# Kernel tuning notes

Hardware: AMD Instinct MI355X
Metric: run time of the kernel (lower is better)

Reference implementation:

```python
import jax, jax.numpy as jnp
import numpy as np

B, C, H, W = 8, 512, 64, 64
NUMS, V_C = 1024, 512
RATE = 0.999


def _normalize(x):
    # matches torch F.normalize(dim=-1, eps=1e-12)
    return x / jnp.clip(jnp.linalg.norm(x, axis=-1, keepdims=True), 1e-12)


def setup_inputs() -> dict:
    key = jax.random.key(0)
    k1, k2, k3 = jax.random.split(key, 3)
    return {
        "x": jax.random.normal(k1, (B, C, H, W), dtype=jnp.float32),
        "noise_feature": jax.random.normal(k2, (NUMS, C), dtype=jnp.float32),
        "std": jax.random.normal(k3, (NUMS, V_C), dtype=jnp.float32),
    }


def reference(x, noise_feature, std):
    b, c, h, w = x.shape
    # (b,c,h,w) -> (n,c)
    xf = jnp.transpose(x, (0, 2, 3, 1)).reshape(-1, c)
    m = jax.lax.stop_gradient(noise_feature)  # torch uses .data (no grad)
    xn = _normalize(xf)
    mn = _normalize(m)
    score = xn @ mn.T  # (n, k) cosine similarities

    # EMA codebook update (training path, update_flag=True)
    xd = jax.lax.stop_gradient(xf)
    embed_ind = jnp.argmax(score, axis=1)  # (n,)
    # segment_sum == x.T @ one_hot(ind), transposed; avoids dense one-hot GEMM
    embed_sum = jax.ops.segment_sum(xd, embed_ind, num_segments=NUMS)  # (k, c)
    counts = jax.ops.segment_sum(jnp.ones((xd.shape[0],), xd.dtype), embed_ind,
                                 num_segments=NUMS)  # (k,)
    embed_mean = embed_sum / (counts[:, None] + 1e-6)
    new_m = m * RATE + embed_mean * (1.0 - RATE)

    mn2 = _normalize(new_m)
    score2 = xn @ mn2.T  # (n, k)
    soft_label = jax.nn.softmax(score2, axis=1)
    out = (soft_label @ std).reshape(b, h, w, V_C)
    return out, score2
```

## Files before the change

kernel.cpp:

```cpp
#include <hip/hip_runtime.h>
#include <stdint.h>

#define NROWS 32768
#define CDIM  512
#define KCODES 1024
#define VC    512
#define LDP 72

typedef unsigned short u16;
typedef unsigned long long u64;
using bf16x8 = __attribute__((ext_vector_type(8))) __bf16;
using f32x4  = __attribute__((ext_vector_type(4))) float;

__device__ __forceinline__ float bf2f(u16 u){
  union { unsigned int i; float f; } x; x.i = ((unsigned int)u) << 16; return x.f;
}
__device__ __forceinline__ u16 f2bf(float f){
  union { float f; unsigned int i; } x; x.f = f;
  unsigned int u = x.i;
  u += 0x7fffu + ((u >> 16) & 1u);
  return (u16)(u >> 16);
}
__device__ __forceinline__ unsigned int pack2(u16 lo, u16 hi){
  return (unsigned int)lo | ((unsigned int)hi << 16);
}
__device__ __forceinline__ unsigned int fkey(float f){
  unsigned int u = __float_as_uint(f);
  return (u & 0x80000000u) ? ~u : (u | 0x80000000u);
}
__device__ __forceinline__ f32x4 mfma16(bf16x8 a, bf16x8 b, f32x4 c){
  return __builtin_amdgcn_mfma_f32_16x16x32_bf16(a, b, c, 0, 0, 0);
}
__device__ __forceinline__ void gload_lds16(const void* g, void* l){
  __builtin_amdgcn_global_load_lds(
      (const __attribute__((address_space(1))) unsigned int*)g,
      (__attribute__((address_space(3))) unsigned int*)l, 16, 0, 0);
}

__global__ __launch_bounds__(256) void k_transpose_x(const float* __restrict__ x,
                                                     u16* __restrict__ xf,
                                                     float* __restrict__ rsum){
  __shared__ float tile[64 * 64];
  int b  = blockIdx.z;
  int p0 = blockIdx.x * 64;
  int c0 = blockIdx.y * 64;
  int t  = threadIdx.x;
  const float* xb = x + (size_t)b * CDIM * 4096 + (size_t)c0 * 4096 + p0;

  int pl4 = (t & 15) * 4;
#pragma unroll
  for (int i = 0; i < 4; i++){
    int cl = i * 16 + (t >> 4);
    float4 v = *(const float4*)(xb + (size_t)cl * 4096 + pl4);
    *(float4*)(tile + cl * 64 + (pl4 ^ (cl & 0x38))) = v;
  }
  __syncthreads();

  int cl0 = (t & 7) * 8;
#pragma unroll
  for (int pass = 0; pass < 2; pass++){
    int pl = pass * 32 + (t >> 3);
    float v[8]; float s = 0.f;
#pragma unroll
    for (int j = 0; j < 8; j++){
      v[j] = tile[(cl0 + j) * 64 + (pl ^ cl0)];
      s += v[j] * v[j];
    }
    uint4 o;
    o.x = pack2(f2bf(v[0]), f2bf(v[1]));
    o.y = pack2(f2bf(v[2]), f2bf(v[3]));
    o.z = pack2(f2bf(v[4]), f2bf(v[5]));
    o.w = pack2(f2bf(v[6]), f2bf(v[7]));
    *(uint4*)(xf + (size_t)(b * 4096 + p0 + pl) * CDIM + c0 + cl0) = o;
    s += __shfl_xor(s, 1, 64);
    s += __shfl_xor(s, 2, 64);
    s += __shfl_xor(s, 4, 64);
    if ((t & 7) == 0) atomicAdd(rsum + b * 4096 + p0 + pl, s);
  }
}

__global__ __launch_bounds__(256) void k_prep(const float* __restrict__ in,
                                              u16* __restrict__ mn,
                                              const float* __restrict__ sd,
                                              u16* __restrict__ stdT){
  int t = threadIdx.x;
  if (blockIdx.x < 256){
    int row  = blockIdx.x * 4 + (t >> 6);
    int lane = t & 63;
    const float* r = in + (size_t)row * CDIM;
    float v[8]; float s = 0.f;
#pragma unroll
    for (int i = 0; i < 8; i++){ v[i] = r[lane + i * 64]; s += v[i] * v[i]; }
#pragma unroll
    for (int off = 32; off; off >>= 1) s += __shfl_xor(s, off, 64);
    float inv = 1.0f / fmaxf(sqrtf(s), 1e-12f);
#pragma unroll
    for (int i = 0; i < 8; i++) mn[(size_t)row * CDIM + lane + i * 64] = f2bf(v[i] * inv);
  } else {
    __shared__ float tile[32][33];
    int bid = blockIdx.x - 256;
    int k0 = (bid & 31) * 32;
    int v0 = (bid >> 5) * 32;
    int tx = t & 31, ty = t >> 5;
#pragma unroll
    for (int i = 0; i < 4; i++)
      tile[ty + i * 8][tx] = sd[(size_t)(k0 + ty + i * 8) * VC + v0 + tx];
    __syncthreads();
#pragma unroll
    for (int i = 0; i < 4; i++)
      stdT[(size_t)(v0 + ty + i * 8) * KCODES + k0 + tx] = f2bf(tile[tx][ty + i * 8]);
  }
}

__global__ __launch_bounds__(512, 4) void k_gemm1_am(const u16* __restrict__ xf,
                                                     const u16* __restrict__ mn,
                                                     u64* __restrict__ packed){
  __shared__ __align__(16) u16 As[256 * 64];
  __shared__ __align__(16) u16 Bs[128 * 64];
  int tid  = threadIdx.x;
  int wave = tid >> 6, lane = tid & 63;
  int wr = wave >> 1, wc = wave & 1;
  int quad = lane >> 4, l15 = lane & 15;
  int c0 = blockIdx.x * 128, r0 = blockIdx.y * 256;

  int srow = lane >> 3, schunk = lane & 7;
  const u16* ag = xf + (size_t)(r0 + wave * 8 + srow) * CDIM + schunk * 8;
  const u16* bg = mn + (size_t)(c0 + wave * 8 + srow) * CDIM + schunk * 8;
  u16* adst = As + wave * 8 * 64;
  u16* bdst = Bs + wave * 8 * 64;

  f32x4 acc[4][4];
#pragma unroll
  for (int rt = 0; rt < 4; rt++)
#pragma unroll
    for (int ct = 0; ct < 4; ct++) acc[rt][ct] = (f32x4)(0.f);

  for (int k0 = 0; k0 < CDIM; k0 += 64){
#pragma unroll
    for (int i = 0; i < 4; i++)
      gload_lds16(ag + (size_t)(i * 64) * CDIM + k0, adst + i * 64 * 64);
#pragma unroll
    for (int j = 0; j < 2; j++)
      gload_lds16(bg + (size_t)(j * 64) * CDIM + k0, bdst + j * 64 * 64);
    __syncthreads();
#pragma unroll
    for (int ks = 0; ks < 2; ks++){
      bf16x8 af[4], bfr[4];
#pragma unroll
      for (int rt = 0; rt < 4; rt++)
        af[rt] = *(const bf16x8*)(As + (wr * 64 + rt * 16 + l15) * 64 + ks * 32 + quad * 8);
#pragma unroll
      for (int ct = 0; ct < 4; ct++)
        bfr[ct] = *(const bf16x8*)(Bs + (wc * 64 + ct * 16 + l15) * 64 + ks * 32 + quad * 8);
#pragma unroll
      for (int rt = 0; rt < 4; rt++)
#pragma unroll
        for (int ct = 0; ct < 4; ct++)
          acc[rt][ct] = mfma16(af[rt], bfr[ct], acc[rt][ct]);
    }
    __syncthreads();
  }

#pragma unroll
  for (int rt = 0; rt < 4; rt++){
#pragma unroll
    for (int q = 0; q < 4; q++){
      float bv = acc[rt][0][q];
      int   bc = c0 + wc * 64 + l15;
#pragma unroll
      for (int ct = 1; ct < 4; ct++){
        float v = acc[rt][ct][q];
        int   c = c0 + wc * 64 + ct * 16 + l15;
        if (v > bv){ bv = v; bc = c; }
      }
#pragma unroll
      for (int off = 1; off <= 8; off <<= 1){
        float ov = __shfl_xor(bv, off, 64);
        int   oc = __shfl_xor(bc, off, 64);
        if (ov > bv || (ov == bv && oc < bc)){ bv = ov; bc = oc; }
      }
      if (l15 == 0){
        int rg = r0 + wr * 64 + rt * 16 + quad * 4 + q;
        u64 key = ((u64)fkey(bv) << 32) | (unsigned int)(~(unsigned int)bc);
        atomicMax(packed + rg, key);
      }
    }
  }
}

__global__ __launch_bounds__(256) void k_gather(const u64* __restrict__ packed,
                                                const u16* __restrict__ xf,
                                                float* __restrict__ esum,
                                                float* __restrict__ counts){
  __shared__ float part[4][CDIM];
  __shared__ int   wcnt[4];
  int code = blockIdx.x;
  int tid = threadIdx.x, wave = tid >> 6, lane = tid & 63;
  float acc[8] = {0,0,0,0,0,0,0,0};
  int cnt = 0;
  for (int base = wave * 64; base < NROWS; base += 256){
    u64 pk = packed[base + lane];
    int cl = (int)(~(unsigned int)(pk & 0xffffffffull)) & (KCODES - 1);
    int match = (cl == code);
    u64 mask = __ballot(match);
    cnt += (int)__popcll(mask);
    while (mask){
      int b = __ffsll((long long)mask) - 1;
      mask &= mask - 1;
      int rr = base + b;
      uint4 v = *(const uint4*)(xf + (size_t)rr * CDIM + lane * 8);
      unsigned int w[4] = {v.x, v.y, v.z, v.w};
#pragma unroll
      for (int i = 0; i < 4; i++){
        acc[2 * i]     += bf2f((u16)(w[i] & 0xffffu));
        acc[2 * i + 1] += bf2f((u16)(w[i] >> 16));
      }
    }
  }
#pragma unroll
  for (int j = 0; j < 8; j++) part[wave][lane * 8 + j] = acc[j];
  if (lane == 0) wcnt[wave] = cnt;
  __syncthreads();
  for (int c = tid; c < CDIM; c += 256)
    esum[(size_t)code * CDIM + c] = part[0][c] + part[1][c] + part[2][c] + part[3][c];
  if (tid == 0) counts[code] = (float)(wcnt[0] + wcnt[1] + wcnt[2] + wcnt[3]);
}

__global__ __launch_bounds__(256) void k_newm(const float* __restrict__ m,
                                              const float* __restrict__ esum,
                                              const float* __restrict__ counts,
                                              u16* __restrict__ mn2){
  int row  = blockIdx.x * 4 + (threadIdx.x >> 6);
  int lane = threadIdx.x & 63;
  float cnt = counts[row];
  float sc  = 0.001f / (cnt + 1e-6f);
  float v[8]; float s = 0.f;
#pragma unroll
  for (int i = 0; i < 8; i++){
    int c = lane + i * 64;
    v[i] = m[(size_t)row * CDIM + c] * 0.999f + esum[(size_t)row * CDIM + c] * sc;
    s += v[i] * v[i];
  }
#pragma unroll
  for (int off = 32; off; off >>= 1) s += __shfl_xor(s, off, 64);
  float inv = 1.0f / fmaxf(sqrtf(s), 1e-12f);
#pragma unroll
  for (int i = 0; i < 8; i++) mn2[(size_t)row * CDIM + lane + i * 64] = f2bf(v[i] * inv);
}

__global__ __launch_bounds__(512, 4) void k_gemm2(const u16* __restrict__ xf,
                                                  const u16* __restrict__ mn2,
                                                  const float* __restrict__ rsum,
                                                  float* __restrict__ score2,
                                                  float* __restrict__ pmax,
                                                  float* __restrict__ psum){
  __shared__ __align__(16) u16 As[256 * 64];
  __shared__ __align__(16) u16 Bs[128 * 64];
  int tid  = threadIdx.x;
  int wave = tid >> 6, lane = tid & 63;
  int wr = wave >> 1, wc = wave & 1;
  int quad = lane >> 4, l15 = lane & 15;
  int c0 = blockIdx.x * 128, r0 = blockIdx.y * 256;

  int srow = lane >> 3, schunk = lane & 7;
  const u16* ag = xf  + (size_t)(r0 + wave * 8 + srow) * CDIM + schunk * 8;
  const u16* bg = mn2 + (size_t)(c0 + wave * 8 + srow) * CDIM + schunk * 8;
  u16* adst = As + wave * 8 * 64;
  u16* bdst = Bs + wave * 8 * 64;

  f32x4 acc[4][4];
#pragma unroll
  for (int rt = 0; rt < 4; rt++)
#pragma unroll
    for (int ct = 0; ct < 4; ct++) acc[rt][ct] = (f32x4)(0.f);

  for (int k0 = 0; k0 < CDIM; k0 += 64){
#pragma unroll
    for (int i = 0; i < 4; i++)
      gload_lds16(ag + (size_t)(i * 64) * CDIM + k0, adst + i * 64 * 64);
#pragma unroll
    for (int j = 0; j < 2; j++)
      gload_lds16(bg + (size_t)(j * 64) * CDIM + k0, bdst + j * 64 * 64);
    __syncthreads();
#pragma unroll
    for (int ks = 0; ks < 2; ks++){
      bf16x8 af[4], bfr[4];
#pragma unroll
      for (int rt = 0; rt < 4; rt++)
        af[rt] = *(const bf16x8*)(As + (wr * 64 + rt * 16 + l15) * 64 + ks * 32 + quad * 8);
#pragma unroll
      for (int ct = 0; ct < 4; ct++)
        bfr[ct] = *(const bf16x8*)(Bs + (wc * 64 + ct * 16 + l15) * 64 + ks * 32 + quad * 8);
#pragma unroll
      for (int rt = 0; rt < 4; rt++)
#pragma unroll
        for (int ct = 0; ct < 4; ct++)
          acc[rt][ct] = mfma16(af[rt], bfr[ct], acc[rt][ct]);
    }
    __syncthreads();
  }

#pragma unroll
  for (int rt = 0; rt < 4; rt++){
#pragma unroll
    for (int q = 0; q < 4; q++){
      int grow = r0 + wr * 64 + rt * 16 + quad * 4 + q;
      float rv = 1.0f / fmaxf(sqrtf(rsum[grow]), 1e-12f);
      float v0 = acc[rt][0][q] * rv;
      float v1 = acc[rt][1][q] * rv;
      float v2 = acc[rt][2][q] * rv;
      float v3 = acc[rt][3][q] * rv;
      float* so = score2 + (size_t)grow * KCODES + c0 + wc * 64 + l15;
      so[0]  = v0;
      so[16] = v1;
      so[32] = v2;
      so[48] = v3;
      float mx = fmaxf(fmaxf(v0, v1), fmaxf(v2, v3));
#pragma unroll
      for (int off = 1; off <= 8; off <<= 1) mx = fmaxf(mx, __shfl_xor(mx, off, 64));
      float s = __expf(v0 - mx) + __expf(v1 - mx) + __expf(v2 - mx) + __expf(v3 - mx);
#pragma unroll
      for (int off = 1; off <= 8; off <<= 1) s += __shfl_xor(s, off, 64);
      if (l15 == 0){
        int pi = grow * 16 + blockIdx.x * 2 + wc;
        pmax[pi] = mx;
        psum[pi] = s;
      }
    }
  }
}

__global__ __launch_bounds__(256) void k_softcomb(const float* __restrict__ pmax,
                                                  const float* __restrict__ psum,
                                                  float* __restrict__ rowmax,
                                                  float* __restrict__ rsinv){
  int row = blockIdx.x * 256 + threadIdx.x;
  const float* pm = pmax + (size_t)row * 16;
  const float* ps = psum + (size_t)row * 16;
  float M = pm[0];
#pragma unroll
  for (int i = 1; i < 16; i++) M = fmaxf(M, pm[i]);
  float S = 0.f;
#pragma unroll
  for (int i = 0; i < 16; i++) S += ps[i] * __expf(pm[i] - M);
  rowmax[row] = M;
  rsinv[row]  = 1.0f / S;
}

__global__ __launch_bounds__(512) void k_gemm3(const float* __restrict__ score2,
                                               const float* __restrict__ rowmax,
                                               const float* __restrict__ rsinv,
                                               const u16* __restrict__ stdT,
                                               float* __restrict__ out){
  __shared__ __align__(16) u16 As[128 * LDP];
  __shared__ __align__(16) u16 Bs[256 * 64];
  int tid  = threadIdx.x;
  int wave = tid >> 6, lane = tid & 63;
  int wr = wave >> 2, wcol = wave & 3;
  int quad = lane >> 4, l15 = lane & 15;
  int c0 = blockIdx.x * 256, r0 = blockIdx.y * 128;
  int arow = tid >> 2, aq = tid & 3;

  int srow = lane >> 3, schunk = lane & 7;
  const u16* bg = stdT + (size_t)(c0 + wave * 8 + srow) * KCODES + schunk * 8;
  u16* bdst = Bs + wave * 8 * 64;

  float rmax = rowmax[r0 + arow];
  float rs   = rsinv [r0 + arow];

  f32x4 acc[4][4];
#pragma unroll
  for (int rt = 0; rt < 4; rt++)
#pragma unroll
    for (int ct = 0; ct < 4; ct++) acc[rt][ct] = (f32x4)(0.f);

  const float* ag = score2 + (size_t)(r0 + arow) * KCODES + aq * 16;

  for (int k0 = 0; k0 < KCODES; k0 += 64){
#pragma unroll
    for (int i = 0; i < 4; i++)
      gload_lds16(bg + (size_t)i * 64 * KCODES + k0, bdst + i * 64 * 64);
#pragma unroll
    for (int j = 0; j < 2; j++){
      float4 a = *(const float4*)(ag + k0 + j * 8);
      float4 b = *(const float4*)(ag + k0 + j * 8 + 4);
      uint4 o;
      o.x = pack2(f2bf(__expf(a.x - rmax) * rs), f2bf(__expf(a.y - rmax) * rs));
      o.y = pack2(f2bf(__expf(a.z - rmax) * rs), f2bf(__expf(a.w - rmax) * rs));
      o.z = pack2(f2bf(__expf(b.x - rmax) * rs), f2bf(__expf(b.y - rmax) * rs));
      o.w = pack2(f2bf(__expf(b.z - rmax) * rs), f2bf(__expf(b.w - rmax) * rs));
      *(uint4*)(As + arow * LDP + aq * 16 + j * 8) = o;
    }
    __syncthreads();
#pragma unroll
    for (int ks = 0; ks < 2; ks++){
      bf16x8 af[4], bfr[4];
#pragma unroll
      for (int rt = 0; rt < 4; rt++)
        af[rt] = *(const bf16x8*)(As + (wr * 64 + rt * 16 + l15) * LDP + ks * 32 + quad * 8);
#pragma unroll
      for (int ct = 0; ct < 4; ct++)
        bfr[ct] = *(const bf16x8*)(Bs + (wcol * 64 + ct * 16 + l15) * 64 + ks * 32 + quad * 8);
#pragma unroll
      for (int rt = 0; rt < 4; rt++)
#pragma unroll
        for (int ct = 0; ct < 4; ct++)
          acc[rt][ct] = mfma16(af[rt], bfr[ct], acc[rt][ct]);
    }
    __syncthreads();
  }
#pragma unroll
  for (int rt = 0; rt < 4; rt++){
#pragma unroll
    for (int q = 0; q < 4; q++){
      int grow = r0 + wr * 64 + rt * 16 + quad * 4 + q;
#pragma unroll
      for (int ct = 0; ct < 4; ct++){
        int gcol = c0 + wcol * 64 + ct * 16 + l15;
        out[(size_t)grow * VC + gcol] = acc[rt][ct][q];
      }
    }
  }
}

extern "C" void kernel_launch(void* const* d_in, const int* in_sizes, int n_in,
                              void* d_out, int out_size, void* d_ws, size_t ws_size,
                              hipStream_t stream){
  (void)in_sizes; (void)n_in; (void)out_size; (void)ws_size;
  const float* x      = (const float*)d_in[0];
  const float* m      = (const float*)d_in[1];
  const float* stdmat = (const float*)d_in[2];
  float* out    = (float*)d_out;
  float* score2 = out + (size_t)NROWS * VC;

  char* ws = (char*)d_ws;
  u16*   xf     = (u16*)  (ws + 0);
  u16*   mn     = (u16*)  (ws + 33554432);
  u16*   mn2    = (u16*)  (ws + 34603008);
  u16*   stdT   = (u16*)  (ws + 35651584);
  u64*   packed = (u64*)  (ws + 36831232);
  float* esum   = (float*)(ws + 37224448);
  float* counts = (float*)(ws + 39321600);
  float* rowmax = (float*)(ws + 39325696);
  float* rsinv  = (float*)(ws + 39456768);
  float* pmax   = (float*)(ws + 39587840);
  float* psum   = (float*)(ws + 41684992);
  float* rsum   = rowmax;

  hipMemsetAsync(packed, 0, (size_t)NROWS * 8, stream);
  hipMemsetAsync(rsum,   0, (size_t)NROWS * 4, stream);

  k_transpose_x  <<<dim3(64, 8, 8), 256, 0, stream>>>(x, xf, rsum);
  k_prep         <<<768, 256, 0, stream>>>(m, mn, stdmat, stdT);
  k_gemm1_am     <<<dim3(KCODES / 128, NROWS / 256), 512, 0, stream>>>(xf, mn, packed);
  k_gather       <<<KCODES, 256, 0, stream>>>(packed, xf, esum, counts);
  k_newm         <<<KCODES / 4, 256, 0, stream>>>(m, esum, counts, mn2);
  k_gemm2        <<<dim3(KCODES / 128, NROWS / 256), 512, 0, stream>>>(xf, mn2, rsum, score2, pmax, psum);
  k_softcomb     <<<NROWS / 256, 256, 0, stream>>>(pmax, psum, rowmax, rsinv);
  k_gemm3        <<<dim3(VC / 256, NROWS / 128), 512, 0, stream>>>(score2, rowmax, rsinv, stdT, out);
}
```

Before: 463.2 us.

## Drop softmax max-subtraction and remap blocks for XCD-aware tile locality

Score2 values are cosine similarities bounded in [-1,1], so the row-max pass is removed. The softmax now exponentiates raw scores, and the 1/sum normalization moves into the GEMM3 epilogue. This removes the pmax buffer, the max shuffles and the per-element subtract and multiply in GEMM3's A-tile conversion. Separately, block IDs in all three GEMMs are remapped so that consecutive blocks, which are spread round-robin across the 8 XCDs, share row tiles for better L2 reuse. The no-max softmax relies on the bounded score range, which holds mathematically for normalized vectors.

```diff
diff --git a/kernel.cpp b/kernel.cpp
--- a/kernel.cpp
+++ b/kernel.cpp
@@ -121,7 +121,10 @@
   int wave = tid >> 6, lane = tid & 63;
   int wr = wave >> 1, wc = wave & 1;
   int quad = lane >> 4, l15 = lane & 15;
-  int c0 = blockIdx.x * 128, r0 = blockIdx.y * 256;
+  int bid  = blockIdx.y * gridDim.x + blockIdx.x;
+  int work = (bid & 7) * 128 + (bid >> 3);
+  int r0 = (work >> 3) * 256;
+  int c0 = (work & 7) * 128;
 
   int srow = lane >> 3, schunk = lane & 7;
   const u16* ag = xf + (size_t)(r0 + wave * 8 + srow) * CDIM + schunk * 8;
@@ -252,7 +255,6 @@
                                                   const u16* __restrict__ mn2,
                                                   const float* __restrict__ rsum,
                                                   float* __restrict__ score2,
-                                                  float* __restrict__ pmax,
                                                   float* __restrict__ psum){
   __shared__ __align__(16) u16 As[256 * 64];
   __shared__ __align__(16) u16 Bs[128 * 64];
@@ -260,7 +262,11 @@
   int wave = tid >> 6, lane = tid & 63;
   int wr = wave >> 1, wc = wave & 1;
   int quad = lane >> 4, l15 = lane & 15;
-  int c0 = blockIdx.x * 128, r0 = blockIdx.y * 256;
+  int bid  = blockIdx.y * gridDim.x + blockIdx.x;
+  int work = (bid & 7) * 128 + (bid >> 3);
+  int r0   = (work >> 3) * 256;
+  int cidx = work & 7;
+  int c0   = cidx * 128;
 
   int srow = lane >> 3, schunk = lane & 7;
   const u16* ag = xf  + (size_t)(r0 + wave * 8 + srow) * CDIM + schunk * 8;
@@ -315,40 +321,25 @@
       so[16] = v1;
       so[32] = v2;
       so[48] = v3;
-      float mx = fmaxf(fmaxf(v0, v1), fmaxf(v2, v3));
-#pragma unroll
-      for (int off = 1; off <= 8; off <<= 1) mx = fmaxf(mx, __shfl_xor(mx, off, 64));
-      float s = __expf(v0 - mx) + __expf(v1 - mx) + __expf(v2 - mx) + __expf(v3 - mx);
-#pragma unroll
-      for (int off = 1; off <= 8; off <<= 1) s += __shfl_xor(s, off, 64);
-      if (l15 == 0){
-        int pi = grow * 16 + blockIdx.x * 2 + wc;
-        pmax[pi] = mx;
-        psum[pi] = s;
-      }
-    }
-  }
-}
-
-__global__ __launch_bounds__(256) void k_softcomb(const float* __restrict__ pmax,
-                                                  const float* __restrict__ psum,
-                                                  float* __restrict__ rowmax,
-                                                  float* __restrict__ rsinv){
+      float ss = __expf(v0) + __expf(v1) + __expf(v2) + __expf(v3);
+#pragma unroll
+      for (int off = 1; off <= 8; off <<= 1) ss += __shfl_xor(ss, off, 64);
+      if (l15 == 0) psum[grow * 16 + cidx * 2 + wc] = ss;
+    }
+  }
+}
+
+__global__ __launch_bounds__(256) void k_rsinv(const float* __restrict__ psum,
+                                               float* __restrict__ rsinv){
   int row = blockIdx.x * 256 + threadIdx.x;
-  const float* pm = pmax + (size_t)row * 16;
   const float* ps = psum + (size_t)row * 16;
-  float M = pm[0];
-#pragma unroll
-  for (int i = 1; i < 16; i++) M = fmaxf(M, pm[i]);
   float S = 0.f;
 #pragma unroll
-  for (int i = 0; i < 16; i++) S += ps[i] * __expf(pm[i] - M);
-  rowmax[row] = M;
-  rsinv[row]  = 1.0f / S;
+  for (int i = 0; i < 16; i++) S += ps[i];
+  rsinv[row] = 1.0f / S;
 }
 
 __global__ __launch_bounds__(512) void k_gemm3(const float* __restrict__ score2,
-                                               const float* __restrict__ rowmax,
                                                const float* __restrict__ rsinv,
                                                const u16* __restrict__ stdT,
                                                float* __restrict__ out){
@@ -358,15 +349,15 @@
   int wave = tid >> 6, lane = tid & 63;
   int wr = wave >> 2, wcol = wave & 3;
   int quad = lane >> 4, l15 = lane & 15;
-  int c0 = blockIdx.x * 256, r0 = blockIdx.y * 128;
+  int bid  = blockIdx.y * gridDim.x + blockIdx.x;
+  int work = (bid & 7) * 64 + (bid >> 3);
+  int r0 = (work >> 1) * 128;
+  int c0 = (work & 1) * 256;
   int arow = tid >> 2, aq = tid & 3;
 
   int srow = lane >> 3, schunk = lane & 7;
   const u16* bg = stdT + (size_t)(c0 + wave * 8 + srow) * KCODES + schunk * 8;
   u16* bdst = Bs + wave * 8 * 64;
-
-  float rmax = rowmax[r0 + arow];
-  float rs   = rsinv [r0 + arow];
 
   f32x4 acc[4][4];
 #pragma unroll
@@ -385,10 +376,10 @@
       float4 a = *(const float4*)(ag + k0 + j * 8);
       float4 b = *(const float4*)(ag + k0 + j * 8 + 4);
       uint4 o;
-      o.x = pack2(f2bf(__expf(a.x - rmax) * rs), f2bf(__expf(a.y - rmax) * rs));
-      o.y = pack2(f2bf(__expf(a.z - rmax) * rs), f2bf(__expf(a.w - rmax) * rs));
-      o.z = pack2(f2bf(__expf(b.x - rmax) * rs), f2bf(__expf(b.y - rmax) * rs));
-      o.w = pack2(f2bf(__expf(b.z - rmax) * rs), f2bf(__expf(b.w - rmax) * rs));
+      o.x = pack2(f2bf(__expf(a.x)), f2bf(__expf(a.y)));
+      o.y = pack2(f2bf(__expf(a.z)), f2bf(__expf(a.w)));
+      o.z = pack2(f2bf(__expf(b.x)), f2bf(__expf(b.y)));
+      o.w = pack2(f2bf(__expf(b.z)), f2bf(__expf(b.w)));
       *(uint4*)(As + arow * LDP + aq * 16 + j * 8) = o;
     }
     __syncthreads();
@@ -414,10 +405,11 @@
 #pragma unroll
     for (int q = 0; q < 4; q++){
       int grow = r0 + wr * 64 + rt * 16 + quad * 4 + q;
+      float rs = rsinv[grow];
 #pragma unroll
       for (int ct = 0; ct < 4; ct++){
         int gcol = c0 + wcol * 64 + ct * 16 + l15;
-        out[(size_t)grow * VC + gcol] = acc[rt][ct][q];
+        out[(size_t)grow * VC + gcol] = acc[rt][ct][q] * rs;
       }
     }
   }
@@ -441,11 +433,9 @@
   u64*   packed = (u64*)  (ws + 36831232);
   float* esum   = (float*)(ws + 37224448);
   float* counts = (float*)(ws + 39321600);
-  float* rowmax = (float*)(ws + 39325696);
+  float* rsum   = (float*)(ws + 39325696);
   float* rsinv  = (float*)(ws + 39456768);
-  float* pmax   = (float*)(ws + 39587840);
   float* psum   = (float*)(ws + 41684992);
-  float* rsum   = rowmax;
 
   hipMemsetAsync(packed, 0, (size_t)NROWS * 8, stream);
   hipMemsetAsync(rsum,   0, (size_t)NROWS * 4, stream);
@@ -455,7 +445,7 @@
   k_gemm1_am     <<<dim3(KCODES / 128, NROWS / 256), 512, 0, stream>>>(xf, mn, packed);
   k_gather       <<<KCODES, 256, 0, stream>>>(packed, xf, esum, counts);
   k_newm         <<<KCODES / 4, 256, 0, stream>>>(m, esum, counts, mn2);
-  k_gemm2        <<<dim3(KCODES / 128, NROWS / 256), 512, 0, stream>>>(xf, mn2, rsum, score2, pmax, psum);
-  k_softcomb     <<<NROWS / 256, 256, 0, stream>>>(pmax, psum, rowmax, rsinv);
-  k_gemm3        <<<dim3(VC / 256, NROWS / 128), 512, 0, stream>>>(score2, rowmax, rsinv, stdT, out);
-}
+  k_gemm2        <<<dim3(KCODES / 128, NROWS / 256), 512, 0, stream>>>(xf, mn2, rsum, score2, psum);
+  k_rsinv        <<<NROWS / 256, 256, 0, stream>>>(psum, rsinv);
+  k_gemm3        <<<dim3(VC / 256, NROWS / 128), 512, 0, stream>>>(score2, rsinv, stdT, out);
+}
```

Measured after the change: 437.3 us. -5.6%, faster.
